# Kernel tuning notes

Hardware: AMD Instinct MI355X
Metric: run time of the kernel (lower is better)

Reference implementation:

```python
import jax, jax.numpy as jnp
import numpy as np

EPS = 1e-5

def _ln(x, g, b):
    m = x.mean(-1, keepdims=True)
    v = x.var(-1, keepdims=True)
    return (x - m) / jnp.sqrt(v + EPS) * g + b

def _dwconv(x, w, b, stride, pad):
    # x: [B,C,H,W], w: [C,1,k,k] depthwise
    C = x.shape[1]
    y = jax.lax.conv_general_dilated(
        x, w, (stride, stride), pad,
        feature_group_count=C,
        dimension_numbers=('NCHW', 'OIHW', 'NCHW'))
    return y + b[None, :, None, None]

def setup_inputs() -> dict:
    key = jax.random.key(0)
    ks = jax.random.split(key, 16)
    B, H, W, C = 8, 64, 64, 256
    N = H * W
    sr = 8
    d = {}
    d['x'] = jax.random.normal(ks[0], (B, N, C), jnp.float32)
    d['q_w'] = jax.random.normal(ks[1], (C, C), jnp.float32) * 0.02
    d['kv1_w'] = jax.random.normal(ks[2], (C, C), jnp.float32) * 0.02
    d['kv2_w'] = jax.random.normal(ks[3], (C, C), jnp.float32) * 0.02
    d['proj_w'] = jax.random.normal(ks[4], (C, C), jnp.float32) * 0.02
    d['proj_b'] = jnp.zeros((C,), jnp.float32)
    k1 = sr // 2
    d['sr1_w'] = jax.random.normal(ks[5], (C, 1, k1, k1), jnp.float32) * np.sqrt(2.0 / (k1 * k1))
    d['sr1_b'] = jnp.zeros((C,), jnp.float32)
    d['sr2_w'] = jax.random.normal(ks[6], (C, 1, sr, sr), jnp.float32) * np.sqrt(2.0 / (sr * sr))
    d['sr2_b'] = jnp.zeros((C,), jnp.float32)
    d['ln1_g'] = jnp.ones((C,), jnp.float32)
    d['ln1_b'] = jnp.zeros((C,), jnp.float32)
    d['ln2_g'] = jnp.ones((C,), jnp.float32)
    d['ln2_b'] = jnp.zeros((C,), jnp.float32)
    d['lc1_w'] = jax.random.normal(ks[7], (C // 2, 1, 3, 3), jnp.float32) * np.sqrt(2.0 / 9.0)
    d['lc1_b'] = jnp.zeros((C // 2,), jnp.float32)
    d['lc2_w'] = jax.random.normal(ks[8], (C // 2, 1, 3, 3), jnp.float32) * np.sqrt(2.0 / 9.0)
    d['lc2_b'] = jnp.zeros((C // 2,), jnp.float32)
    d['H'] = H
    d['W'] = W
    return d

def reference(x, q_w, kv1_w, kv2_w, proj_w, proj_b,
              sr1_w, sr1_b, sr2_w, sr2_b,
              ln1_g, ln1_b, ln2_g, ln2_b,
              lc1_w, lc1_b, lc2_w, lc2_b, H, W):
    B, N, C = x.shape
    nh = 8
    nh2 = nh // 2
    hd = C // nh
    sr = 8
    scale = hd ** -0.5

    # q: [B, nh, N, hd]
    q = jnp.einsum('bnc,dc->bnd', x, q_w).reshape(B, N, nh, hd).transpose(0, 2, 1, 3)

    x_ = x.transpose(0, 2, 1).reshape(B, C, H, W)
    x1 = _dwconv(x_, sr1_w, sr1_b, sr // 2, 'VALID')            # [B,C,H/4,W/4]
    x1 = x1.reshape(B, C, -1).transpose(0, 2, 1)                 # [B,N1,C]
    x1 = jax.nn.gelu(_ln(x1, ln1_g, ln1_b), approximate=False)
    x2 = _dwconv(x_, sr2_w, sr2_b, sr, 'VALID')                  # [B,C,H/8,W/8]
    x2 = x2.reshape(B, C, -1).transpose(0, 2, 1)                 # [B,N2,C]
    x2 = jax.nn.gelu(_ln(x2, ln2_g, ln2_b), approximate=False)

    def branch(xr, kv_w, qh, Hs, Ws, lc_w, lc_b):
        Bn, Ns, _ = xr.shape
        kv = jnp.einsum('bnc,dc->bnd', xr, kv_w).reshape(Bn, Ns, 2, nh2, hd).transpose(2, 0, 3, 1, 4)
        k, v = kv[0], kv[1]                                      # [B,nh2,Ns,hd]
        attn = jax.nn.softmax(jnp.einsum('bhqd,bhkd->bhqk', qh, k) * scale, axis=-1)
        # depthwise local conv injected into v
        v_sp = v.transpose(0, 2, 1, 3).reshape(Bn, Ns, C // 2).transpose(0, 2, 1).reshape(Bn, C // 2, Hs, Ws)
        v_lc = _dwconv(v_sp, lc_w, lc_b, 1, ((1, 1), (1, 1)))
        v = v + v_lc.reshape(Bn, nh2, hd, Ns).transpose(0, 1, 3, 2)
        out = jnp.einsum('bhqk,bhkd->bhqd', attn, v)             # [B,nh2,N,hd]
        return out.transpose(0, 2, 1, 3).reshape(Bn, N, C // 2)

    o1 = branch(x1, kv1_w, q[:, :nh2], H * 2 // sr, W * 2 // sr, lc1_w, lc1_b)
    o2 = branch(x2, kv2_w, q[:, nh2:], H // sr, W // sr, lc2_w, lc2_b)
    out = jnp.concatenate([o1, o2], axis=-1)
    return jnp.einsum('bnc,dc->bnd', out, proj_w) + proj_b
```

## Files before the change

kernel.cpp:

```cpp
#include <hip/hip_runtime.h>
#include <math.h>

static constexpr int Bb  = 8;
static constexpr int Nn  = 4096;
static constexpr int Cc  = 256;
static constexpr int N1c = 256;
static constexpr int N2c = 64;

typedef __attribute__((ext_vector_type(8))) _Float16 f16x8;
typedef __attribute__((ext_vector_type(4))) _Float16 f16x4;
typedef __attribute__((ext_vector_type(4))) float    f32x4v;

__global__ __launch_bounds__(256)
void prep(const float* __restrict__ w0, const float* __restrict__ w1,
          const float* __restrict__ w2, const float* __restrict__ w3,
          const float* __restrict__ sr1w, const float* __restrict__ sr2w,
          _Float16* __restrict__ wf, float* __restrict__ wt1, float* __restrict__ wt2) {
  const int bid = blockIdx.x, c = threadIdx.x;
  if (bid < 256) {
    const int wsel = bid >> 6;
    const float* w = wsel == 0 ? w0 : wsel == 1 ? w1 : wsel == 2 ? w2 : w3;
    const int i = ((bid & 63) * 256 + c) * 4;
    float4 v = *(const float4*)(w + i);
    f16x4 o = {(_Float16)v.x, (_Float16)v.y, (_Float16)v.z, (_Float16)v.w};
    *(f16x4*)(wf + (size_t)wsel * 65536 + i) = o;
  } else {
    const int row = bid - 256;
    if (row < 16) wt1[row * 256 + c] = sr1w[c * 16 + row];
    else { const int q = row - 16; wt2[q * 256 + c] = sr2w[c * 64 + q]; }
  }
}

template<bool A_HALF, bool OUT_HALF, bool BIAS>
__device__ __forceinline__
void gemm_body(const void* __restrict__ Ain, const _Float16* __restrict__ Wf,
               const float* __restrict__ bias, void* __restrict__ Outv, int m0) {
  __shared__ _Float16 Asl[2][64][40];
  __shared__ _Float16 Bsl[2][256][40];
  const int tid = threadIdx.x, lane = tid & 63, wid = tid >> 6;
  const int qi = lane & 15, g = lane >> 4;
  const int ar = tid >> 2, ak = (tid & 3) * 8;

  const float*    pa32 = (const float*)Ain    + (size_t)(m0 + ar) * 256 + ak;
  const _Float16* pa16 = (const _Float16*)Ain + (size_t)(m0 + ar) * 256 + ak;
  const _Float16* pw   = Wf + (size_t)tid * 256;

  f32x4v acc[4][4] = {};
  f16x8 rA; f16x8 rB[4];

#define LDREG(k0)                                                        \
  do {                                                                   \
    if (A_HALF) {                                                        \
      rA = *(const f16x8*)(pa16 + (k0));                                 \
    } else {                                                             \
      float4 t0 = *(const float4*)(pa32 + (k0));                         \
      float4 t1 = *(const float4*)(pa32 + (k0) + 4);                     \
      rA = (f16x8){(_Float16)t0.x, (_Float16)t0.y, (_Float16)t0.z,       \
                   (_Float16)t0.w, (_Float16)t1.x, (_Float16)t1.y,       \
                   (_Float16)t1.z, (_Float16)t1.w};                      \
    }                                                                    \
    _Pragma("unroll")                                                    \
    for (int i = 0; i < 4; ++i) rB[i] = *(const f16x8*)(pw + (k0) + i * 8); \
  } while (0)

#define DSWRITE(buf)                                                     \
  do {                                                                   \
    *(f16x8*)&Asl[buf][ar][ak] = rA;                                     \
    _Pragma("unroll")                                                    \
    for (int i = 0; i < 4; ++i) *(f16x8*)&Bsl[buf][tid][i * 8] = rB[i];  \
  } while (0)

  LDREG(0);
  DSWRITE(0);
  LDREG(32);
  __syncthreads();

#pragma unroll
  for (int ks = 0; ks < 8; ++ks) {
    const int cur = ks & 1;
    if (ks < 7) DSWRITE(cur ^ 1);
    if (ks < 6) LDREG((ks + 2) * 32);
    f16x8 af[4], bf[4];
#pragma unroll
    for (int mt = 0; mt < 4; ++mt)
      af[mt] = *(const f16x8*)&Asl[cur][mt * 16 + qi][g * 8];
#pragma unroll
    for (int nt = 0; nt < 4; ++nt)
      bf[nt] = *(const f16x8*)&Bsl[cur][wid * 64 + nt * 16 + qi][g * 8];
#pragma unroll
    for (int nt = 0; nt < 4; ++nt)
#pragma unroll
      for (int mt = 0; mt < 4; ++mt)
        acc[mt][nt] = __builtin_amdgcn_mfma_f32_16x16x32_f16(af[mt], bf[nt], acc[mt][nt], 0, 0, 0);
    __syncthreads();
  }
#undef LDREG
#undef DSWRITE

#pragma unroll
  for (int nt = 0; nt < 4; ++nt) {
    const int col = wid * 64 + nt * 16 + qi;
    const float bv = BIAS ? bias[col] : 0.f;
#pragma unroll
    for (int mt = 0; mt < 4; ++mt) {
#pragma unroll
      for (int r = 0; r < 4; ++r) {
        const int row = m0 + mt * 16 + g * 4 + r;
        if (OUT_HALF)
          ((_Float16*)Outv)[(size_t)row * 256 + col] = (_Float16)acc[mt][nt][r];
        else
          ((float*)Outv)[(size_t)row * 256 + col] = acc[mt][nt][r] + bv;
      }
    }
  }
}

template<bool A_HALF, bool OUT_HALF, bool BIAS>
__global__ __launch_bounds__(256)
void gemm_lds(const void* __restrict__ Ain, const _Float16* __restrict__ Wf,
              const float* __restrict__ bias, void* __restrict__ Outv) {
  gemm_body<A_HALF, OUT_HALF, BIAS>(Ain, Wf, bias, Outv, blockIdx.x * 64);
}

__global__ __launch_bounds__(256)
void gemm_kv(const _Float16* __restrict__ A1, const _Float16* __restrict__ A2,
             const _Float16* __restrict__ W1, const _Float16* __restrict__ W2,
             _Float16* __restrict__ O1, _Float16* __restrict__ O2) {
  const int bx = blockIdx.x;
  if (bx < 32) gemm_body<true, true, false>(A1, W1, nullptr, O1, bx * 64);
  else         gemm_body<true, true, false>(A2, W2, nullptr, O2, (bx - 32) * 64);
}

__global__ __launch_bounds__(256)
void down2_ln_gelu(const float* __restrict__ x,
                   const float* __restrict__ wt1, const float* __restrict__ b1,
                   const float* __restrict__ g1, const float* __restrict__ lb1,
                   const float* __restrict__ wt2, const float* __restrict__ b2,
                   const float* __restrict__ g2, const float* __restrict__ lb2,
                   _Float16* __restrict__ x1o, _Float16* __restrict__ x2o) {
  const int b = blockIdx.y;
  const int n2 = blockIdx.x;
  const int i2 = n2 >> 3, j2 = n2 & 7;
  const int c = threadIdx.x;
  const int lane = c & 63, wave = c >> 6;
  const float* xb = x + ((size_t)b * Nn) * Cc + c;

  float w1r[16];
#pragma unroll
  for (int t = 0; t < 16; ++t) w1r[t] = wt1[t * 256 + c];

  float a2 = b2[c];
  float a1[2][2] = {{b1[c], b1[c]}, {b1[c], b1[c]}};
#pragma unroll
  for (int dy = 0; dy < 8; ++dy) {
    float vr[8], w2r[8];
#pragma unroll
    for (int dx = 0; dx < 8; ++dx) {
      vr[dx]  = xb[(size_t)((8 * i2 + dy) * 64 + 8 * j2 + dx) * 256];
      w2r[dx] = wt2[(dy * 8 + dx) * 256 + c];
    }
#pragma unroll
    for (int dx = 0; dx < 8; ++dx) {
      a2 = fmaf(w2r[dx], vr[dx], a2);
      a1[dy >> 2][dx >> 2] = fmaf(w1r[(dy & 3) * 4 + (dx & 3)], vr[dx],
                                  a1[dy >> 2][dx >> 2]);
    }
  }

  float vals[5] = {a2, a1[0][0], a1[0][1], a1[1][0], a1[1][1]};
  __shared__ float redS[4][5], redQ[4][5];
  float sum[5], sq[5];
#pragma unroll
  for (int p = 0; p < 5; ++p) {
    float s = vals[p], q2 = vals[p] * vals[p];
#pragma unroll
    for (int off = 1; off < 64; off <<= 1) {
      s  += __shfl_xor(s, off);
      q2 += __shfl_xor(q2, off);
    }
    if (lane == 0) { redS[wave][p] = s; redQ[wave][p] = q2; }
  }
  __syncthreads();
#pragma unroll
  for (int p = 0; p < 5; ++p) {
    sum[p] = redS[0][p] + redS[1][p] + redS[2][p] + redS[3][p];
    sq[p]  = redQ[0][p] + redQ[1][p] + redQ[2][p] + redQ[3][p];
  }
#pragma unroll
  for (int p = 0; p < 5; ++p) {
    const float mean = sum[p] * (1.f / Cc);
    const float var  = sq[p] * (1.f / Cc) - mean * mean;
    const float gg = (p == 0) ? g2[c] : g1[c];
    const float bb = (p == 0) ? lb2[c] : lb1[c];
    const float xn = (vals[p] - mean) * rsqrtf(var + 1e-5f) * gg + bb;
    const float gel = 0.5f * xn * (1.f + erff(xn * 0.70710678118654752440f));
    if (p == 0) {
      x2o[((size_t)b * N2c + n2) * 256 + c] = (_Float16)gel;
    } else {
      const int a = (p - 1) >> 1, bbx = (p - 1) & 1;
      const int n1 = (2 * i2 + a) * 16 + (2 * j2 + bbx);
      x1o[((size_t)b * N1c + n1) * 256 + c] = (_Float16)gel;
    }
  }
}

template<int HS>
__device__ __forceinline__
void vconv_body(const _Float16* __restrict__ kv, const float* __restrict__ w,
                const float* __restrict__ bias, _Float16* __restrict__ vo,
                int b, int n1, int c) {
  constexpr int NS = HS * HS;
  const int i = n1 / HS, j = n1 % HS;
  const _Float16* vb = kv + ((size_t)b * NS) * 256 + 128 + c;
  const float* wc = w + c * 9;
  float acc = bias[c];
#pragma unroll
  for (int dy = 0; dy < 3; ++dy) {
    const int ii = i + dy - 1;
    if (ii < 0 || ii >= HS) continue;
#pragma unroll
    for (int dx = 0; dx < 3; ++dx) {
      const int jj = j + dx - 1;
      if (jj < 0 || jj >= HS) continue;
      acc = fmaf(wc[dy * 3 + dx], (float)vb[(size_t)(ii * HS + jj) * 256], acc);
    }
  }
  vo[((size_t)b * NS + n1) * 128 + c] = (_Float16)(acc + (float)vb[(size_t)n1 * 256]);
}

__global__ __launch_bounds__(128)
void vconv2(const _Float16* __restrict__ kv1, const _Float16* __restrict__ kv2,
            const float* __restrict__ w1, const float* __restrict__ b1,
            const float* __restrict__ w2, const float* __restrict__ b2,
            _Float16* __restrict__ vn1, _Float16* __restrict__ vn2) {
  const int bid = blockIdx.x, c = threadIdx.x;
  if (bid < 2048) vconv_body<16>(kv1, w1, b1, vn1, bid >> 8, bid & 255, c);
  else { const int t = bid - 2048; vconv_body<8>(kv2, w2, b2, vn2, t >> 6, t & 63, c); }
}

template<int NS>
__global__ __launch_bounds__(256, 2)
void attn_f16(_Float16* __restrict__ qo, const _Float16* __restrict__ kv,
              const _Float16* __restrict__ vnew, const int branch) {
  constexpr int NT = NS / 16, NC = NS / 32, PS = NS + 8;
  constexpr float KC = 0.17677669529663688f * 1.4426950408889634f;
  __shared__ _Float16 Klds[NS][40];
  __shared__ _Float16 Vt[32][PS];
  __shared__ _Float16 Pl[64][PS];

  const int tid = threadIdx.x, lane = tid & 63, wid = tid >> 6;
  const int g = lane >> 4, qi = lane & 15;
  const int h = blockIdx.y, b = blockIdx.z;
  const int ck = h * 32;
  const int cq = branch * 128 + h * 32;

  for (int r = tid; r < NS; r += 256) {
    const _Float16* kp = kv   + ((size_t)(b * NS + r)) * 256 + ck;
    const _Float16* vp = vnew + ((size_t)(b * NS + r)) * 128 + ck;
#pragma unroll
    for (int i = 0; i < 4; ++i)
      *(f16x8*)&Klds[r][8 * i] = *(const f16x8*)(kp + 8 * i);
    _Float16 va[32];
#pragma unroll
    for (int i = 0; i < 4; ++i)
      *(f16x8*)&va[8 * i] = *(const f16x8*)(vp + 8 * i);
#pragma unroll
    for (int d = 0; d < 32; ++d) Vt[d][r] = va[d];
  }
  __syncthreads();

  f16x8 vt[2][NC];
#pragma unroll
  for (int dt = 0; dt < 2; ++dt)
#pragma unroll
    for (int c = 0; c < NC; ++c)
      vt[dt][c] = *(const f16x8*)&Vt[16 * dt + qi][32 * c + 8 * g];

  _Float16* Pw = &Pl[wid * 16 + qi][0];

  for (int qt = 0; qt < 4; ++qt) {
    const int qrow = blockIdx.x * 256 + wid * 64 + qt * 16 + qi;
    _Float16* qp = qo + ((size_t)b * Nn + qrow) * 256 + cq;
    f16x8 qfrag = *(const f16x8*)(qp + 8 * g);
    f32x4v s[NT];
#pragma unroll
    for (int t = 0; t < NT; ++t) {
      f16x8 kf = *(const f16x8*)&Klds[16 * t + qi][8 * g];
      s[t] = __builtin_amdgcn_mfma_f32_16x16x32_f16(kf, qfrag,
                                                    (f32x4v){0.f, 0.f, 0.f, 0.f}, 0, 0, 0);
    }
    float m = s[0][0];
#pragma unroll
    for (int t = 0; t < NT; ++t)
      m = fmaxf(m, fmaxf(fmaxf(s[t][0], s[t][1]), fmaxf(s[t][2], s[t][3])));
    m = fmaxf(m, __shfl_xor(m, 16));
    m = fmaxf(m, __shfl_xor(m, 32));
    float l = 0.f;
#pragma unroll
    for (int t = 0; t < NT; ++t)
#pragma unroll
      for (int r = 0; r < 4; ++r) {
        float p = exp2f((s[t][r] - m) * KC);
        s[t][r] = p; l += p;
      }
    l += __shfl_xor(l, 16);
    l += __shfl_xor(l, 32);
#pragma unroll
    for (int t = 0; t < NT; ++t) {
      f16x4 pw = {(_Float16)s[t][0], (_Float16)s[t][1],
                  (_Float16)s[t][2], (_Float16)s[t][3]};
      *(f16x4*)&Pw[16 * t + 4 * g] = pw;
    }
    f32x4v o0 = {0.f, 0.f, 0.f, 0.f}, o1 = {0.f, 0.f, 0.f, 0.f};
#pragma unroll
    for (int c = 0; c < NC; ++c) {
      f16x8 pf = *(const f16x8*)&Pw[32 * c + 8 * g];
      o0 = __builtin_amdgcn_mfma_f32_16x16x32_f16(vt[0][c], pf, o0, 0, 0, 0);
      o1 = __builtin_amdgcn_mfma_f32_16x16x32_f16(vt[1][c], pf, o1, 0, 0, 0);
    }
    const float inv = 1.f / l;
    f16x4 O0 = {(_Float16)(o0[0] * inv), (_Float16)(o0[1] * inv),
                (_Float16)(o0[2] * inv), (_Float16)(o0[3] * inv)};
    f16x4 O1 = {(_Float16)(o1[0] * inv), (_Float16)(o1[1] * inv),
                (_Float16)(o1[2] * inv), (_Float16)(o1[3] * inv)};
    *(f16x4*)(qp + 4 * g)      = O0;
    *(f16x4*)(qp + 16 + 4 * g) = O1;
  }
}

extern "C" void kernel_launch(void* const* d_in, const int* in_sizes, int n_in,
                              void* d_out, int out_size, void* d_ws, size_t ws_size,
                              hipStream_t stream) {
  const float* x      = (const float*)d_in[0];
  const float* q_w    = (const float*)d_in[1];
  const float* kv1_w  = (const float*)d_in[2];
  const float* kv2_w  = (const float*)d_in[3];
  const float* proj_w = (const float*)d_in[4];
  const float* proj_b = (const float*)d_in[5];
  const float* sr1_w  = (const float*)d_in[6];
  const float* sr1_b  = (const float*)d_in[7];
  const float* sr2_w  = (const float*)d_in[8];
  const float* sr2_b  = (const float*)d_in[9];
  const float* ln1_g  = (const float*)d_in[10];
  const float* ln1_b  = (const float*)d_in[11];
  const float* ln2_g  = (const float*)d_in[12];
  const float* ln2_b  = (const float*)d_in[13];
  const float* lc1_w  = (const float*)d_in[14];
  const float* lc1_b  = (const float*)d_in[15];
  const float* lc2_w  = (const float*)d_in[16];
  const float* lc2_b  = (const float*)d_in[17];
  float* out = (float*)d_out;

  char* wsb = (char*)d_ws;
  _Float16* wf   = (_Float16*)wsb;
  _Float16* qh   = wf + (size_t)4 * 65536;
  _Float16* x1h  = qh + (size_t)Bb * Nn * Cc;
  _Float16* x2h  = x1h + (size_t)Bb * N1c * Cc;
  _Float16* kv1h = x2h + (size_t)Bb * N2c * Cc;
  _Float16* kv2h = kv1h + (size_t)Bb * N1c * Cc;
  _Float16* vn1h = kv2h + (size_t)Bb * N2c * Cc;
  _Float16* vn2h = vn1h + (size_t)Bb * N1c * 128;
  float* wt1 = (float*)(vn2h + (size_t)Bb * N2c * 128);
  float* wt2 = wt1 + 16 * 256;

  prep<<<336, 256, 0, stream>>>(q_w, kv1_w, kv2_w, proj_w, sr1_w, sr2_w, wf, wt1, wt2);
  gemm_lds<false, true, false><<<512, 256, 0, stream>>>(x, wf, nullptr, qh);
  down2_ln_gelu<<<dim3(64, Bb), 256, 0, stream>>>(x, wt1, sr1_b, ln1_g, ln1_b,
                                                  wt2, sr2_b, ln2_g, ln2_b, x1h, x2h);
  gemm_kv<<<40, 256, 0, stream>>>(x1h, x2h, wf + 65536, wf + 2 * 65536, kv1h, kv2h);
  vconv2<<<2560, 128, 0, stream>>>(kv1h, kv2h, lc1_w, lc1_b, lc2_w, lc2_b, vn1h, vn2h);
  attn_f16<256><<<dim3(16, 4, Bb), 256, 0, stream>>>(qh, kv1h, vn1h, 0);
  attn_f16<64> <<<dim3(16, 4, Bb), 256, 0, stream>>>(qh, kv2h, vn2h, 1);
  gemm_lds<true, false, true><<<512, 256, 0, stream>>>(qh, wf + 3 * 65536, proj_b, out);
}
```

Before: 89.52 us.

## Fuse pipeline into four kernels with head-major Q/KV layout and in-attention vconv

Merges the weight prep with the downsample+LN+GELU kernel, which now reads the conv weights directly with vector loads instead of a transposed copy. The Q and both KV projections run in one launch, and the separate attention launches plus the vconv kernel become a single kernel that computes the depthwise local conv in shared memory. Q and KV are written in a head-major [B,head,N,32] layout so attention reads contiguous rows, and the projection GEMM gathers from that layout. This cuts the launch count from eight to four and removes the intermediate vnew buffers. The cost is a larger shared-memory footprint in the attention kernel and strided A loads in the projection GEMM.

```diff
diff --git a/kernel.cpp b/kernel.cpp
--- a/kernel.cpp
+++ b/kernel.cpp
@@ -12,10 +12,15 @@
 typedef __attribute__((ext_vector_type(4))) float    f32x4v;
 
 __global__ __launch_bounds__(256)
-void prep(const float* __restrict__ w0, const float* __restrict__ w1,
-          const float* __restrict__ w2, const float* __restrict__ w3,
-          const float* __restrict__ sr1w, const float* __restrict__ sr2w,
-          _Float16* __restrict__ wf, float* __restrict__ wt1, float* __restrict__ wt2) {
+void prep_down(const float* __restrict__ w0, const float* __restrict__ w1,
+               const float* __restrict__ w2, const float* __restrict__ w3,
+               const float* __restrict__ x,
+               const float* __restrict__ sr1w, const float* __restrict__ b1,
+               const float* __restrict__ g1,   const float* __restrict__ lb1,
+               const float* __restrict__ sr2w, const float* __restrict__ b2,
+               const float* __restrict__ g2,   const float* __restrict__ lb2,
+               _Float16* __restrict__ wf, _Float16* __restrict__ x1o,
+               _Float16* __restrict__ x2o) {
   const int bid = blockIdx.x, c = threadIdx.x;
   if (bid < 256) {
     const int wsel = bid >> 6;
@@ -24,141 +29,29 @@
     float4 v = *(const float4*)(w + i);
     f16x4 o = {(_Float16)v.x, (_Float16)v.y, (_Float16)v.z, (_Float16)v.w};
     *(f16x4*)(wf + (size_t)wsel * 65536 + i) = o;
-  } else {
-    const int row = bid - 256;
-    if (row < 16) wt1[row * 256 + c] = sr1w[c * 16 + row];
-    else { const int q = row - 16; wt2[q * 256 + c] = sr2w[c * 64 + q]; }
-  }
-}
-
-template<bool A_HALF, bool OUT_HALF, bool BIAS>
-__device__ __forceinline__
-void gemm_body(const void* __restrict__ Ain, const _Float16* __restrict__ Wf,
-               const float* __restrict__ bias, void* __restrict__ Outv, int m0) {
-  __shared__ _Float16 Asl[2][64][40];
-  __shared__ _Float16 Bsl[2][256][40];
-  const int tid = threadIdx.x, lane = tid & 63, wid = tid >> 6;
-  const int qi = lane & 15, g = lane >> 4;
-  const int ar = tid >> 2, ak = (tid & 3) * 8;
-
-  const float*    pa32 = (const float*)Ain    + (size_t)(m0 + ar) * 256 + ak;
-  const _Float16* pa16 = (const _Float16*)Ain + (size_t)(m0 + ar) * 256 + ak;
-  const _Float16* pw   = Wf + (size_t)tid * 256;
-
-  f32x4v acc[4][4] = {};
-  f16x8 rA; f16x8 rB[4];
-
-#define LDREG(k0)                                                        \
-  do {                                                                   \
-    if (A_HALF) {                                                        \
-      rA = *(const f16x8*)(pa16 + (k0));                                 \
-    } else {                                                             \
-      float4 t0 = *(const float4*)(pa32 + (k0));                         \
-      float4 t1 = *(const float4*)(pa32 + (k0) + 4);                     \
-      rA = (f16x8){(_Float16)t0.x, (_Float16)t0.y, (_Float16)t0.z,       \
-                   (_Float16)t0.w, (_Float16)t1.x, (_Float16)t1.y,       \
-                   (_Float16)t1.z, (_Float16)t1.w};                      \
-    }                                                                    \
-    _Pragma("unroll")                                                    \
-    for (int i = 0; i < 4; ++i) rB[i] = *(const f16x8*)(pw + (k0) + i * 8); \
-  } while (0)
-
-#define DSWRITE(buf)                                                     \
-  do {                                                                   \
-    *(f16x8*)&Asl[buf][ar][ak] = rA;                                     \
-    _Pragma("unroll")                                                    \
-    for (int i = 0; i < 4; ++i) *(f16x8*)&Bsl[buf][tid][i * 8] = rB[i];  \
-  } while (0)
-
-  LDREG(0);
-  DSWRITE(0);
-  LDREG(32);
-  __syncthreads();
-
-#pragma unroll
-  for (int ks = 0; ks < 8; ++ks) {
-    const int cur = ks & 1;
-    if (ks < 7) DSWRITE(cur ^ 1);
-    if (ks < 6) LDREG((ks + 2) * 32);
-    f16x8 af[4], bf[4];
-#pragma unroll
-    for (int mt = 0; mt < 4; ++mt)
-      af[mt] = *(const f16x8*)&Asl[cur][mt * 16 + qi][g * 8];
-#pragma unroll
-    for (int nt = 0; nt < 4; ++nt)
-      bf[nt] = *(const f16x8*)&Bsl[cur][wid * 64 + nt * 16 + qi][g * 8];
-#pragma unroll
-    for (int nt = 0; nt < 4; ++nt)
-#pragma unroll
-      for (int mt = 0; mt < 4; ++mt)
-        acc[mt][nt] = __builtin_amdgcn_mfma_f32_16x16x32_f16(af[mt], bf[nt], acc[mt][nt], 0, 0, 0);
-    __syncthreads();
-  }
-#undef LDREG
-#undef DSWRITE
-
-#pragma unroll
-  for (int nt = 0; nt < 4; ++nt) {
-    const int col = wid * 64 + nt * 16 + qi;
-    const float bv = BIAS ? bias[col] : 0.f;
-#pragma unroll
-    for (int mt = 0; mt < 4; ++mt) {
-#pragma unroll
-      for (int r = 0; r < 4; ++r) {
-        const int row = m0 + mt * 16 + g * 4 + r;
-        if (OUT_HALF)
-          ((_Float16*)Outv)[(size_t)row * 256 + col] = (_Float16)acc[mt][nt][r];
-        else
-          ((float*)Outv)[(size_t)row * 256 + col] = acc[mt][nt][r] + bv;
-      }
-    }
-  }
-}
-
-template<bool A_HALF, bool OUT_HALF, bool BIAS>
-__global__ __launch_bounds__(256)
-void gemm_lds(const void* __restrict__ Ain, const _Float16* __restrict__ Wf,
-              const float* __restrict__ bias, void* __restrict__ Outv) {
-  gemm_body<A_HALF, OUT_HALF, BIAS>(Ain, Wf, bias, Outv, blockIdx.x * 64);
-}
-
-__global__ __launch_bounds__(256)
-void gemm_kv(const _Float16* __restrict__ A1, const _Float16* __restrict__ A2,
-             const _Float16* __restrict__ W1, const _Float16* __restrict__ W2,
-             _Float16* __restrict__ O1, _Float16* __restrict__ O2) {
-  const int bx = blockIdx.x;
-  if (bx < 32) gemm_body<true, true, false>(A1, W1, nullptr, O1, bx * 64);
-  else         gemm_body<true, true, false>(A2, W2, nullptr, O2, (bx - 32) * 64);
-}
-
-__global__ __launch_bounds__(256)
-void down2_ln_gelu(const float* __restrict__ x,
-                   const float* __restrict__ wt1, const float* __restrict__ b1,
-                   const float* __restrict__ g1, const float* __restrict__ lb1,
-                   const float* __restrict__ wt2, const float* __restrict__ b2,
-                   const float* __restrict__ g2, const float* __restrict__ lb2,
-                   _Float16* __restrict__ x1o, _Float16* __restrict__ x2o) {
-  const int b = blockIdx.y;
-  const int n2 = blockIdx.x;
+    return;
+  }
+  const int t = bid - 256;
+  const int b = t >> 6, n2 = t & 63;
   const int i2 = n2 >> 3, j2 = n2 & 7;
-  const int c = threadIdx.x;
   const int lane = c & 63, wave = c >> 6;
   const float* xb = x + ((size_t)b * Nn) * Cc + c;
 
   float w1r[16];
 #pragma unroll
-  for (int t = 0; t < 16; ++t) w1r[t] = wt1[t * 256 + c];
+  for (int q = 0; q < 4; ++q)
+    *(float4*)&w1r[4 * q] = *(const float4*)(sr1w + c * 16 + 4 * q);
 
   float a2 = b2[c];
   float a1[2][2] = {{b1[c], b1[c]}, {b1[c], b1[c]}};
 #pragma unroll
   for (int dy = 0; dy < 8; ++dy) {
     float vr[8], w2r[8];
-#pragma unroll
-    for (int dx = 0; dx < 8; ++dx) {
-      vr[dx]  = xb[(size_t)((8 * i2 + dy) * 64 + 8 * j2 + dx) * 256];
-      w2r[dx] = wt2[(dy * 8 + dx) * 256 + c];
-    }
+    *(float4*)&w2r[0] = *(const float4*)(sr2w + c * 64 + dy * 8);
+    *(float4*)&w2r[4] = *(const float4*)(sr2w + c * 64 + dy * 8 + 4);
+#pragma unroll
+    for (int dx = 0; dx < 8; ++dx)
+      vr[dx] = xb[(size_t)((8 * i2 + dy) * 64 + 8 * j2 + dx) * 256];
 #pragma unroll
     for (int dx = 0; dx < 8; ++dx) {
       a2 = fmaf(w2r[dx], vr[dx], a2);
@@ -166,10 +59,8 @@
                                   a1[dy >> 2][dx >> 2]);
     }
   }
-
   float vals[5] = {a2, a1[0][0], a1[0][1], a1[1][0], a1[1][1]};
   __shared__ float redS[4][5], redQ[4][5];
-  float sum[5], sq[5];
 #pragma unroll
   for (int p = 0; p < 5; ++p) {
     float s = vals[p], q2 = vals[p] * vals[p];
@@ -183,13 +74,10 @@
   __syncthreads();
 #pragma unroll
   for (int p = 0; p < 5; ++p) {
-    sum[p] = redS[0][p] + redS[1][p] + redS[2][p] + redS[3][p];
-    sq[p]  = redQ[0][p] + redQ[1][p] + redQ[2][p] + redQ[3][p];
-  }
-#pragma unroll
-  for (int p = 0; p < 5; ++p) {
-    const float mean = sum[p] * (1.f / Cc);
-    const float var  = sq[p] * (1.f / Cc) - mean * mean;
+    const float sum = redS[0][p] + redS[1][p] + redS[2][p] + redS[3][p];
+    const float sq  = redQ[0][p] + redQ[1][p] + redQ[2][p] + redQ[3][p];
+    const float mean = sum * (1.f / Cc);
+    const float var  = sq * (1.f / Cc) - mean * mean;
     const float gg = (p == 0) ? g2[c] : g1[c];
     const float bb = (p == 0) ? lb2[c] : lb1[c];
     const float xn = (vals[p] - mean) * rsqrtf(var + 1e-5f) * gg + bb;
@@ -204,68 +92,172 @@
   }
 }
 
-template<int HS>
+struct GemmSmem { _Float16 Asl[2][64][40]; _Float16 Bsl[2][256][40]; };
+
+template<int AM, int OM, bool BIAS>
 __device__ __forceinline__
-void vconv_body(const _Float16* __restrict__ kv, const float* __restrict__ w,
-                const float* __restrict__ bias, _Float16* __restrict__ vo,
-                int b, int n1, int c) {
-  constexpr int NS = HS * HS;
-  const int i = n1 / HS, j = n1 % HS;
-  const _Float16* vb = kv + ((size_t)b * NS) * 256 + 128 + c;
-  const float* wc = w + c * 9;
-  float acc = bias[c];
-#pragma unroll
-  for (int dy = 0; dy < 3; ++dy) {
-    const int ii = i + dy - 1;
-    if (ii < 0 || ii >= HS) continue;
-#pragma unroll
-    for (int dx = 0; dx < 3; ++dx) {
-      const int jj = j + dx - 1;
-      if (jj < 0 || jj >= HS) continue;
-      acc = fmaf(wc[dy * 3 + dx], (float)vb[(size_t)(ii * HS + jj) * 256], acc);
-    }
-  }
-  vo[((size_t)b * NS + n1) * 128 + c] = (_Float16)(acc + (float)vb[(size_t)n1 * 256]);
-}
-
-__global__ __launch_bounds__(128)
-void vconv2(const _Float16* __restrict__ kv1, const _Float16* __restrict__ kv2,
-            const float* __restrict__ w1, const float* __restrict__ b1,
-            const float* __restrict__ w2, const float* __restrict__ b2,
-            _Float16* __restrict__ vn1, _Float16* __restrict__ vn2) {
-  const int bid = blockIdx.x, c = threadIdx.x;
-  if (bid < 2048) vconv_body<16>(kv1, w1, b1, vn1, bid >> 8, bid & 255, c);
-  else { const int t = bid - 2048; vconv_body<8>(kv2, w2, b2, vn2, t >> 6, t & 63, c); }
-}
-
-template<int NS>
-__global__ __launch_bounds__(256, 2)
-void attn_f16(_Float16* __restrict__ qo, const _Float16* __restrict__ kv,
-              const _Float16* __restrict__ vnew, const int branch) {
+void gemm_body(GemmSmem& sm, const void* __restrict__ Ain,
+               const _Float16* __restrict__ Wf, const float* __restrict__ bias,
+               void* __restrict__ Outv, int m0) {
+  const int tid = threadIdx.x, lane = tid & 63, wid = tid >> 6;
+  const int qi = lane & 15, g = lane >> 4;
+  const int ar = tid >> 2, ak = (tid & 3) * 8;
+  const int arow = m0 + ar;
+
+  const float*    pa32 = (const float*)Ain + (size_t)arow * 256 + ak;
+  const _Float16* pa16f = (const _Float16*)Ain + (size_t)arow * 256 + ak;
+  const _Float16* pa16h = (const _Float16*)Ain
+      + ((size_t)(arow >> 12) * 8 * 4096 + (arow & 4095)) * 32 + ak;
+  const _Float16* pw = Wf + (size_t)tid * 256;
+
+  f32x4v acc[4][4] = {};
+  f16x8 rA; f16x8 rB[4];
+
+#define LDREG(k0)                                                          \
+  do {                                                                     \
+    if (AM == 0) {                                                         \
+      float4 t0 = *(const float4*)(pa32 + (k0));                           \
+      float4 t1 = *(const float4*)(pa32 + (k0) + 4);                       \
+      rA = (f16x8){(_Float16)t0.x, (_Float16)t0.y, (_Float16)t0.z,         \
+                   (_Float16)t0.w, (_Float16)t1.x, (_Float16)t1.y,         \
+                   (_Float16)t1.z, (_Float16)t1.w};                        \
+    } else if (AM == 1) {                                                  \
+      rA = *(const f16x8*)(pa16f + (k0));                                  \
+    } else {                                                               \
+      rA = *(const f16x8*)(pa16h + (size_t)((k0) >> 5) * 131072);          \
+    }                                                                      \
+    _Pragma("unroll")                                                      \
+    for (int i = 0; i < 4; ++i) rB[i] = *(const f16x8*)(pw + (k0) + i * 8);\
+  } while (0)
+
+#define DSWRITE(buf)                                                       \
+  do {                                                                     \
+    *(f16x8*)&sm.Asl[buf][ar][ak] = rA;                                    \
+    _Pragma("unroll")                                                      \
+    for (int i = 0; i < 4; ++i) *(f16x8*)&sm.Bsl[buf][tid][i * 8] = rB[i]; \
+  } while (0)
+
+  LDREG(0);
+  DSWRITE(0);
+  LDREG(32);
+  __syncthreads();
+
+#pragma unroll
+  for (int ks = 0; ks < 8; ++ks) {
+    const int cur = ks & 1;
+    if (ks < 7) DSWRITE(cur ^ 1);
+    if (ks < 6) LDREG((ks + 2) * 32);
+    f16x8 af[4], bf[4];
+#pragma unroll
+    for (int mt = 0; mt < 4; ++mt)
+      af[mt] = *(const f16x8*)&sm.Asl[cur][mt * 16 + qi][g * 8];
+#pragma unroll
+    for (int nt = 0; nt < 4; ++nt)
+      bf[nt] = *(const f16x8*)&sm.Bsl[cur][wid * 64 + nt * 16 + qi][g * 8];
+#pragma unroll
+    for (int nt = 0; nt < 4; ++nt)
+#pragma unroll
+      for (int mt = 0; mt < 4; ++mt)
+        acc[mt][nt] = __builtin_amdgcn_mfma_f32_16x16x32_f16(af[mt], bf[nt], acc[mt][nt], 0, 0, 0);
+    __syncthreads();
+  }
+#undef LDREG
+#undef DSWRITE
+
+#pragma unroll
+  for (int nt = 0; nt < 4; ++nt) {
+    const int col = wid * 64 + nt * 16 + qi;
+    const float bv = BIAS ? bias[col] : 0.f;
+    const int hs = col >> 5, d = col & 31;
+#pragma unroll
+    for (int mt = 0; mt < 4; ++mt) {
+#pragma unroll
+      for (int r = 0; r < 4; ++r) {
+        const int row = m0 + mt * 16 + g * 4 + r;
+        const float v = acc[mt][nt][r];
+        if (OM == 0) {
+          ((float*)Outv)[(size_t)row * 256 + col] = v + bv;
+        } else if (OM == 1) {
+          ((_Float16*)Outv)[((size_t)((row >> 12) * 8 + hs) * 4096 + (row & 4095)) * 32 + d] = (_Float16)v;
+        } else if (OM == 2) {
+          ((_Float16*)Outv)[((size_t)((row >> 8) * 8 + hs) * 256 + (row & 255)) * 32 + d] = (_Float16)v;
+        } else {
+          ((_Float16*)Outv)[((size_t)((row >> 6) * 8 + hs) * 64 + (row & 63)) * 32 + d] = (_Float16)v;
+        }
+      }
+    }
+  }
+}
+
+__global__ __launch_bounds__(256)
+void gemms_qkv(const float* __restrict__ x, const _Float16* __restrict__ x1h,
+               const _Float16* __restrict__ x2h, const _Float16* __restrict__ wf,
+               _Float16* __restrict__ qh, _Float16* __restrict__ kv1,
+               _Float16* __restrict__ kv2) {
+  __shared__ GemmSmem sm;
+  const int bx = blockIdx.x;
+  if (bx < 512)      gemm_body<0, 1, false>(sm, x,   wf,             nullptr, qh,  bx * 64);
+  else if (bx < 544) gemm_body<1, 2, false>(sm, x1h, wf + 65536,     nullptr, kv1, (bx - 512) * 64);
+  else               gemm_body<1, 3, false>(sm, x2h, wf + 2 * 65536, nullptr, kv2, (bx - 544) * 64);
+}
+
+__global__ __launch_bounds__(256)
+void gemm_proj(const _Float16* __restrict__ qh, const _Float16* __restrict__ wf,
+               const float* __restrict__ bias, float* __restrict__ out) {
+  __shared__ GemmSmem sm;
+  gemm_body<2, 0, true>(sm, qh, wf, bias, out, blockIdx.x * 64);
+}
+
+template<int NS, int HS>
+__device__ __forceinline__
+void attn_body(char* smem, _Float16* __restrict__ qh, const _Float16* __restrict__ kvh,
+               const float* __restrict__ lcw, const float* __restrict__ lcb,
+               int qc, int b, int h, int hg) {
   constexpr int NT = NS / 16, NC = NS / 32, PS = NS + 8;
   constexpr float KC = 0.17677669529663688f * 1.4426950408889634f;
-  __shared__ _Float16 Klds[NS][40];
-  __shared__ _Float16 Vt[32][PS];
-  __shared__ _Float16 Pl[64][PS];
+  _Float16 (*Klds)[40] = (_Float16(*)[40])smem;
+  _Float16 (*Vt)[PS]   = (_Float16(*)[PS])(smem + (size_t)NS * 40 * 2);
+  _Float16* PlBase     = (_Float16*)(smem + (size_t)NS * 40 * 2 + (size_t)32 * PS * 2);
+  _Float16 (*vraw)[32] = (_Float16(*)[32])PlBase;
 
   const int tid = threadIdx.x, lane = tid & 63, wid = tid >> 6;
   const int g = lane >> 4, qi = lane & 15;
-  const int h = blockIdx.y, b = blockIdx.z;
-  const int ck = h * 32;
-  const int cq = branch * 128 + h * 32;
-
+
+  const _Float16* kp0 = kvh + ((size_t)(b * 8 + h) * NS) * 32;
+  const _Float16* vp0 = kvh + ((size_t)(b * 8 + 4 + h) * NS) * 32;
   for (int r = tid; r < NS; r += 256) {
-    const _Float16* kp = kv   + ((size_t)(b * NS + r)) * 256 + ck;
-    const _Float16* vp = vnew + ((size_t)(b * NS + r)) * 128 + ck;
 #pragma unroll
     for (int i = 0; i < 4; ++i)
-      *(f16x8*)&Klds[r][8 * i] = *(const f16x8*)(kp + 8 * i);
-    _Float16 va[32];
+      *(f16x8*)&Klds[r][8 * i] = *(const f16x8*)(kp0 + (size_t)r * 32 + 8 * i);
 #pragma unroll
     for (int i = 0; i < 4; ++i)
-      *(f16x8*)&va[8 * i] = *(const f16x8*)(vp + 8 * i);
-#pragma unroll
-    for (int d = 0; d < 32; ++d) Vt[d][r] = va[d];
+      *(f16x8*)&vraw[r][8 * i] = *(const f16x8*)(vp0 + (size_t)r * 32 + 8 * i);
+  }
+  __syncthreads();
+
+  {
+    const int d = tid & 31, rg = tid >> 5;
+    const int cc = h * 32 + d;
+    float wreg[9];
+#pragma unroll
+    for (int q = 0; q < 9; ++q) wreg[q] = lcw[cc * 9 + q];
+    const float bv = lcb[cc];
+    for (int r0 = rg; r0 < NS; r0 += 8) {
+      const int i = r0 / HS, j = r0 % HS;
+      float acc = bv;
+#pragma unroll
+      for (int dy = 0; dy < 3; ++dy) {
+        const int ii = i + dy - 1;
+        if (ii < 0 || ii >= HS) continue;
+#pragma unroll
+        for (int dx = 0; dx < 3; ++dx) {
+          const int jj = j + dx - 1;
+          if (jj < 0 || jj >= HS) continue;
+          acc = fmaf(wreg[dy * 3 + dx], (float)vraw[ii * HS + jj][d], acc);
+        }
+      }
+      Vt[d][r0] = (_Float16)((float)vraw[r0][d] + acc);
+    }
   }
   __syncthreads();
 
@@ -276,11 +268,12 @@
     for (int c = 0; c < NC; ++c)
       vt[dt][c] = *(const f16x8*)&Vt[16 * dt + qi][32 * c + 8 * g];
 
-  _Float16* Pw = &Pl[wid * 16 + qi][0];
+  _Float16* Pw = PlBase + (size_t)(wid * 16 + qi) * PS;
+  _Float16* qbase = qh + ((size_t)(b * 8 + hg) * 4096) * 32;
 
   for (int qt = 0; qt < 4; ++qt) {
-    const int qrow = blockIdx.x * 256 + wid * 64 + qt * 16 + qi;
-    _Float16* qp = qo + ((size_t)b * Nn + qrow) * 256 + cq;
+    const int qrow = qc * 256 + wid * 64 + qt * 16 + qi;
+    _Float16* qp = qbase + (size_t)qrow * 32;
     f16x8 qfrag = *(const f16x8*)(qp + 8 * g);
     f32x4v s[NT];
 #pragma unroll
@@ -326,6 +319,19 @@
     *(f16x4*)(qp + 4 * g)      = O0;
     *(f16x4*)(qp + 16 + 4 * g) = O1;
   }
+}
+
+__global__ __launch_bounds__(256, 2)
+void attn_all(_Float16* __restrict__ qh,
+              const _Float16* __restrict__ kv1, const _Float16* __restrict__ kv2,
+              const float* __restrict__ lc1w, const float* __restrict__ lc1b,
+              const float* __restrict__ lc2w, const float* __restrict__ lc2b) {
+  __shared__ __align__(16) char smem[71168];
+  const int z = blockIdx.z;
+  const int b = z >> 1, br = z & 1;
+  const int h = blockIdx.y;
+  if (br == 0) attn_body<256, 16>(smem, qh, kv1, lc1w, lc1b, blockIdx.x, b, h, h);
+  else         attn_body<64,  8>(smem, qh, kv2, lc2w, lc2b, blockIdx.x, b, h, 4 + h);
 }
 
 extern "C" void kernel_launch(void* const* d_in, const int* in_sizes, int n_in,
@@ -351,25 +357,19 @@
   const float* lc2_b  = (const float*)d_in[17];
   float* out = (float*)d_out;
 
-  char* wsb = (char*)d_ws;
-  _Float16* wf   = (_Float16*)wsb;
+  _Float16* wf   = (_Float16*)d_ws;
   _Float16* qh   = wf + (size_t)4 * 65536;
   _Float16* x1h  = qh + (size_t)Bb * Nn * Cc;
   _Float16* x2h  = x1h + (size_t)Bb * N1c * Cc;
   _Float16* kv1h = x2h + (size_t)Bb * N2c * Cc;
   _Float16* kv2h = kv1h + (size_t)Bb * N1c * Cc;
-  _Float16* vn1h = kv2h + (size_t)Bb * N2c * Cc;
-  _Float16* vn2h = vn1h + (size_t)Bb * N1c * 128;
-  float* wt1 = (float*)(vn2h + (size_t)Bb * N2c * 128);
-  float* wt2 = wt1 + 16 * 256;
-
-  prep<<<336, 256, 0, stream>>>(q_w, kv1_w, kv2_w, proj_w, sr1_w, sr2_w, wf, wt1, wt2);
-  gemm_lds<false, true, false><<<512, 256, 0, stream>>>(x, wf, nullptr, qh);
-  down2_ln_gelu<<<dim3(64, Bb), 256, 0, stream>>>(x, wt1, sr1_b, ln1_g, ln1_b,
-                                                  wt2, sr2_b, ln2_g, ln2_b, x1h, x2h);
-  gemm_kv<<<40, 256, 0, stream>>>(x1h, x2h, wf + 65536, wf + 2 * 65536, kv1h, kv2h);
-  vconv2<<<2560, 128, 0, stream>>>(kv1h, kv2h, lc1_w, lc1_b, lc2_w, lc2_b, vn1h, vn2h);
-  attn_f16<256><<<dim3(16, 4, Bb), 256, 0, stream>>>(qh, kv1h, vn1h, 0);
-  attn_f16<64> <<<dim3(16, 4, Bb), 256, 0, stream>>>(qh, kv2h, vn2h, 1);
-  gemm_lds<true, false, true><<<512, 256, 0, stream>>>(qh, wf + 3 * 65536, proj_b, out);
-}
+
+  prep_down<<<768, 256, 0, stream>>>(q_w, kv1_w, kv2_w, proj_w, x,
+                                     sr1_w, sr1_b, ln1_g, ln1_b,
+                                     sr2_w, sr2_b, ln2_g, ln2_b,
+                                     wf, x1h, x2h);
+  gemms_qkv<<<552, 256, 0, stream>>>(x, x1h, x2h, wf, qh, kv1h, kv2h);
+  attn_all<<<dim3(16, 4, 16), 256, 0, stream>>>(qh, kv1h, kv2h,
+                                                lc1_w, lc1_b, lc2_w, lc2_b);
+  gemm_proj<<<512, 256, 0, stream>>>(qh, wf + 3 * 65536, proj_b, out);
+}
```

Result: slower. 106.1 us (median of 4 runs) (+18.5%).
